# Kernel optimization log

Hardware: AMD Instinct MI355X
Metric: run time of the kernel (lower is better)

The kernel has to match this reference:

```python
import jax, jax.numpy as jnp
import numpy as np

N_ATOMS = 50000
N_PAIRS = 1000000
F = 64   # per-atom features
G = 16   # radial basis functions
V = 32   # vector features
H1 = 128
IN_F = F + V + 1 + V  # 129, non-first interaction module
OUT_F = F + 2


def setup_inputs() -> dict:
    key = jax.random.key(0)
    ks = jax.random.split(key, 12)
    return {
        "atomic_embedding": jax.random.normal(ks[0], (N_ATOMS, F), dtype=jnp.float32),
        "partial_charges": jax.random.normal(ks[1], (N_ATOMS, 1), dtype=jnp.float32),
        "gs": jax.random.uniform(ks[2], (N_PAIRS, G), dtype=jnp.float32),
        "gv": jax.random.normal(ks[3], (N_PAIRS, 3, G), dtype=jnp.float32),
        "agh": jax.random.normal(ks[4], (F, G, V), dtype=jnp.float32) * (1.0 / np.sqrt(G)),
        "W1": jax.random.normal(ks[5], (IN_F, H1), dtype=jnp.float32) * (1.0 / np.sqrt(IN_F)),
        "b1": jnp.zeros((H1,), dtype=jnp.float32),
        "W2": jax.random.normal(ks[6], (H1, H1), dtype=jnp.float32) * (1.0 / np.sqrt(H1)),
        "b2": jnp.zeros((H1,), dtype=jnp.float32),
        "W3": jax.random.normal(ks[7], (H1, OUT_F), dtype=jnp.float32) * (1.0 / np.sqrt(H1)),
        "b3": jnp.zeros((OUT_F,), dtype=jnp.float32),
        "pair_indices": jax.random.randint(ks[8], (2, N_PAIRS), 0, N_ATOMS, dtype=jnp.int64),
    }


def _interaction(atomic_embedding, partial_charges, gs, gv, agh,
                 W1, b1, W2, b2, W3, b3, idx_j):
    n_atoms = atomic_embedding.shape[0]
    v = agh.shape[-1]

    # --- embedding branch ---
    a_j = atomic_embedding[idx_j]                      # (P, F) gather
    # torch: (gs[:,:,None] * a_j[:,None,:]).sum(1) == gs.sum(1, keepdims) * a_j
    avf_s = jnp.einsum('pg,pf->pf', gs, a_j)           # (P, F)
    radial_emb = jax.ops.segment_sum(avf_s, idx_j, num_segments=n_atoms)  # (N, F)

    avf_v = jnp.einsum('pa,pdg,agh->phd', a_j, gv, agh)  # (P, V, 3)
    vec_emb = jax.ops.segment_sum(jnp.sum(avf_v * avf_v, axis=-1),
                                  idx_j, num_segments=n_atoms)            # (N, V)

    # --- partial-charge branch (agh=None path) ---
    q_j = partial_charges[idx_j]                       # (P, 1)
    avf_s_q = jnp.einsum('pg,pf->pf', gs, q_j)         # (P, 1)
    radial_q = jax.ops.segment_sum(avf_s_q, idx_j, num_segments=n_atoms)  # (N, 1)
    vec_q = jnp.zeros((n_atoms, v), dtype=atomic_embedding.dtype)         # (N, V)

    msg = jnp.concatenate([radial_emb, vec_emb, radial_q, vec_q], axis=1)  # (N, F+V+1+V)

    h = jax.nn.gelu(msg @ W1 + b1, approximate=False)
    h = jax.nn.gelu(h @ W2 + b2, approximate=False)
    out = h @ W3 + b3                                   # (N, F+2)

    delta_q = out[:, 0:1]
    f = out[:, 1:2]
    delta_a = out[:, 2:]
    return delta_a, delta_q, f


def reference(atomic_embedding, partial_charges, gs, gv, agh,
              W1, b1, W2, b2, W3, b3, pair_indices):
    idx_j = pair_indices[1]
    return _interaction(atomic_embedding, partial_charges, gs, gv, agh,
                        W1, b1, W2, b2, W3, b3, idx_j)
```

## Files before the change

### kernel.cpp

```cpp
#include <hip/hip_runtime.h>
#include <math.h>

#define NA 50000
#define NP 1000000
#define OUTF 66
#define SCAN_BLOCKS 196
#define ATB 16
#define TSTR 516


__global__ void k_hist(const int* __restrict__ idxj, int* __restrict__ cnt) {
    int p = blockIdx.x * 256 + threadIdx.x;
    if (p < NP) atomicAdd(&cnt[idxj[p]], 1);
}

__global__ __launch_bounds__(256) void k_scanA(const int* __restrict__ cnt,
                                               int* __restrict__ blkS) {
    __shared__ int sh[256];
    int t = threadIdx.x;
    int i = blockIdx.x * 256 + t;
    sh[t] = (i < NA) ? cnt[i] : 0;
    __syncthreads();
    for (int d = 128; d > 0; d >>= 1) {
        if (t < d) sh[t] += sh[t + d];
        __syncthreads();
    }
    if (t == 0) blkS[blockIdx.x] = sh[0];
}

__global__ __launch_bounds__(256) void k_scanB(int* __restrict__ blkS) {
    __shared__ int sh[256];
    int t = threadIdx.x;
    sh[t] = (t < SCAN_BLOCKS) ? blkS[t] : 0;
    __syncthreads();
    for (int d = 1; d < 256; d <<= 1) {
        int x = (t >= d) ? sh[t - d] : 0;
        __syncthreads();
        sh[t] += x;
        __syncthreads();
    }
    int e = (t == 0) ? 0 : sh[t - 1];
    if (t < SCAN_BLOCKS) blkS[t] = e;
}

__global__ __launch_bounds__(256) void k_scanC(const int* __restrict__ cnt,
                                               const int* __restrict__ blkS,
                                               int* __restrict__ offs,
                                               int* __restrict__ curs) {
    __shared__ int sh[256];
    int t = threadIdx.x;
    int i = blockIdx.x * 256 + t;
    sh[t] = (i < NA) ? cnt[i] : 0;
    __syncthreads();
    for (int d = 1; d < 256; d <<= 1) {
        int x = (t >= d) ? sh[t - d] : 0;
        __syncthreads();
        sh[t] += x;
        __syncthreads();
    }
    int excl = ((t == 0) ? 0 : sh[t - 1]) + blkS[blockIdx.x];
    if (i < NA) { offs[i] = excl; curs[i] = excl; }
}

__global__ void k_scatter(const int* __restrict__ idxj, int* __restrict__ curs,
                          int* __restrict__ sortedP) {
    int p = blockIdx.x * 256 + threadIdx.x;
    if (p < NP) {
        int i = idxj[p];
        int pos = atomicAdd(&curs[i], 1);
        sortedP[pos] = (p << 4) | (i & 15);
    }
}

__global__ __launch_bounds__(256)
void k_atoms(const float* __restrict__ emb,
             const float* __restrict__ agh,
             const float* __restrict__ gs,
             const float* __restrict__ gv,
             const int* __restrict__ sortedP,
             const int* __restrict__ offs,
             float* __restrict__ S,
             float* __restrict__ vec) {
    __shared__ float T_lds[ATB * TSTR];
    __shared__ float embS[ATB * 64];
    __shared__ float vecS[ATB * 33];
    __shared__ float sS[ATB];
    const int t = threadIdx.x;
    const int atom0 = blockIdx.x * ATB;

    for (int k = t; k < ATB * 33; k += 256) vecS[k] = 0.f;
    if (t < ATB) sS[t] = 0.f;
    for (int k = t; k < ATB * 64; k += 256) embS[k] = emb[(size_t)atom0 * 64 + k];
    __syncthreads();

    {
        float acc0[ATB], acc1[ATB];
#pragma unroll
        for (int at = 0; at < ATB; ++at) { acc0[at] = 0.f; acc1[at] = 0.f; }
        const int c0 = t, c1 = t + 256;
        for (int a = 0; a < 64; ++a) {
            float w0 = agh[a * 512 + c0];
            float w1 = agh[a * 512 + c1];
#pragma unroll
            for (int at = 0; at < ATB; ++at) {
                float e = embS[at * 64 + a];
                acc0[at] += e * w0;
                acc1[at] += e * w1;
            }
        }
        const int g0 = c0 >> 5, h0 = c0 & 31;
        const int g1 = c1 >> 5, h1 = c1 & 31;
#pragma unroll
        for (int at = 0; at < ATB; ++at) {
            T_lds[at * TSTR + h0 * 16 + g0] = acc0[at];
            T_lds[at * TSTR + h1 * 16 + g1] = acc1[at];
        }
    }
    __syncthreads();

    const int lane = t & 63;
    const int start = offs[atom0];
    const int end = (blockIdx.x + 1 < 3125) ? offs[atom0 + ATB] : NP;

    for (int kb = start; kb < end; kb += 256) {
        const int k = kb + t;
        const bool ok = (k < end);
        const int pk = ok ? sortedP[k] : 0;
        const int p = ok ? (pk >> 4) : 0;
        const int at = pk & 15;
        const int atm = ok ? at : (64 + lane);

        const int atn = __shfl_xor(atm, 1);
        const bool same = (atn == atm);
        const bool flush = (!same) || ((lane & 1) == 0);

        const float4* gs4 = (const float4*)(gs + (size_t)p * 16);
        float4 sa = gs4[0], sb = gs4[1], sc = gs4[2], sd = gs4[3];
        float gq = (sa.x + sa.y + sa.z + sa.w) + (sb.x + sb.y + sb.z + sb.w) +
                   (sc.x + sc.y + sc.z + sc.w) + (sd.x + sd.y + sd.z + sd.w);
        float gqn = __shfl_xor(gq, 1);
        float gqm = gq + (same ? gqn : 0.f);
        if (ok && flush) atomicAdd(&sS[at], gqm);

        const float* Tb = &T_lds[at * TSTR];
        const float* gvp = gv + (size_t)p * 48;

#pragma unroll 1
        for (int hb = 0; hb < 4; ++hb) {
            float e[8];
#pragma unroll
            for (int x = 0; x < 8; ++x) e[x] = 0.f;

#pragma unroll 1
            for (int d = 0; d < 3; ++d) {
                const float4* gd = (const float4*)(gvp + d * 16);
                float4 g0 = gd[0], g1 = gd[1], g2 = gd[2], g3 = gd[3];
#pragma unroll
                for (int hh = 0; hh < 8; ++hh) {
                    const float4* Tr = (const float4*)(Tb + (hb * 8 + hh) * 16);
                    float4 t0 = Tr[0], t1 = Tr[1], t2 = Tr[2], t3 = Tr[3];
                    float v;
                    v  = g0.x * t0.x; v += g0.y * t0.y;
                    v += g0.z * t0.z; v += g0.w * t0.w;
                    v += g1.x * t1.x; v += g1.y * t1.y;
                    v += g1.z * t1.z; v += g1.w * t1.w;
                    v += g2.x * t2.x; v += g2.y * t2.y;
                    v += g2.z * t2.z; v += g2.w * t2.w;
                    v += g3.x * t3.x; v += g3.y * t3.y;
                    v += g3.z * t3.z; v += g3.w * t3.w;
                    e[hh] += v * v;
                }
            }

#pragma unroll
            for (int hh = 0; hh < 8; ++hh) {
                float en = __shfl_xor(e[hh], 1);
                float em = e[hh] + (same ? en : 0.f);
                if (ok && flush) atomicAdd(&vecS[at * 33 + hb * 8 + hh], em);
            }
        }
    }
    __syncthreads();

    for (int k = t; k < ATB * 32; k += 256) {
        int a = k >> 5, h = k & 31;
        vec[(size_t)(atom0 + a) * 32 + h] = vecS[a * 33 + h];
    }
    if (t < ATB) S[atom0 + t] = sS[t];
}

#define MSTR 132
__global__ __launch_bounds__(256) void k_mlp(const float* __restrict__ emb,
                                             const float* __restrict__ q,
                                             const float* __restrict__ S,
                                             const float* __restrict__ vec,
                                             const float* __restrict__ W1,
                                             const float* __restrict__ b1,
                                             const float* __restrict__ W2,
                                             const float* __restrict__ b2,
                                             const float* __restrict__ W3,
                                             const float* __restrict__ b3,
                                             float* __restrict__ out) {
    __shared__ float bufA[64 * MSTR];
    __shared__ float bufB[64 * MSTR];
    const int t = threadIdx.x;
    const int atom0 = blockIdx.x * 64;

    for (int k = t; k < 64 * 97; k += 256) {
        int a = k / 97, c = k - a * 97;
        int i = atom0 + a;
        float val = 0.f;
        if (i < NA) {
            float s = S[i];
            if (c < 64) val = emb[(size_t)i * 64 + c] * s;
            else if (c < 96) val = vec[(size_t)i * 32 + (c - 64)];
            else val = q[i] * s;
        }
        bufA[a * MSTR + c] = val;
    }
    __syncthreads();

    const int jg = t & 31, ag = t >> 5;
    const int j0 = 4 * jg;
    const int abase = ag * 8;
    float acc[8][4];

    {
        float4 bb = *(const float4*)&b1[j0];
#pragma unroll
        for (int a = 0; a < 8; ++a) {
            acc[a][0] = bb.x; acc[a][1] = bb.y; acc[a][2] = bb.z; acc[a][3] = bb.w;
        }
        for (int k4 = 0; k4 < 96; k4 += 4) {
            float4 w0 = *(const float4*)&W1[(k4 + 0) * 128 + j0];
            float4 w1 = *(const float4*)&W1[(k4 + 1) * 128 + j0];
            float4 w2 = *(const float4*)&W1[(k4 + 2) * 128 + j0];
            float4 w3 = *(const float4*)&W1[(k4 + 3) * 128 + j0];
#pragma unroll
            for (int a = 0; a < 8; ++a) {
                float4 m = *(const float4*)&bufA[(abase + a) * MSTR + k4];
                acc[a][0] += m.x * w0.x + m.y * w1.x + m.z * w2.x + m.w * w3.x;
                acc[a][1] += m.x * w0.y + m.y * w1.y + m.z * w2.y + m.w * w3.y;
                acc[a][2] += m.x * w0.z + m.y * w1.z + m.z * w2.z + m.w * w3.z;
                acc[a][3] += m.x * w0.w + m.y * w1.w + m.z * w2.w + m.w * w3.w;
            }
        }
        {
            float4 w = *(const float4*)&W1[96 * 128 + j0];
#pragma unroll
            for (int a = 0; a < 8; ++a) {
                float m = bufA[(abase + a) * MSTR + 96];
                acc[a][0] += m * w.x; acc[a][1] += m * w.y;
                acc[a][2] += m * w.z; acc[a][3] += m * w.w;
            }
        }
#pragma unroll
        for (int a = 0; a < 8; ++a) {
            float4 o;
            o.x = 0.5f * acc[a][0] * (1.f + erff(acc[a][0] * 0.70710678118654752f));
            o.y = 0.5f * acc[a][1] * (1.f + erff(acc[a][1] * 0.70710678118654752f));
            o.z = 0.5f * acc[a][2] * (1.f + erff(acc[a][2] * 0.70710678118654752f));
            o.w = 0.5f * acc[a][3] * (1.f + erff(acc[a][3] * 0.70710678118654752f));
            *(float4*)&bufB[(abase + a) * MSTR + j0] = o;
        }
    }
    __syncthreads();

    {
        float4 bb = *(const float4*)&b2[j0];
#pragma unroll
        for (int a = 0; a < 8; ++a) {
            acc[a][0] = bb.x; acc[a][1] = bb.y; acc[a][2] = bb.z; acc[a][3] = bb.w;
        }
        for (int k4 = 0; k4 < 128; k4 += 4) {
            float4 w0 = *(const float4*)&W2[(k4 + 0) * 128 + j0];
            float4 w1 = *(const float4*)&W2[(k4 + 1) * 128 + j0];
            float4 w2 = *(const float4*)&W2[(k4 + 2) * 128 + j0];
            float4 w3 = *(const float4*)&W2[(k4 + 3) * 128 + j0];
#pragma unroll
            for (int a = 0; a < 8; ++a) {
                float4 m = *(const float4*)&bufB[(abase + a) * MSTR + k4];
                acc[a][0] += m.x * w0.x + m.y * w1.x + m.z * w2.x + m.w * w3.x;
                acc[a][1] += m.x * w0.y + m.y * w1.y + m.z * w2.y + m.w * w3.y;
                acc[a][2] += m.x * w0.z + m.y * w1.z + m.z * w2.z + m.w * w3.z;
                acc[a][3] += m.x * w0.w + m.y * w1.w + m.z * w2.w + m.w * w3.w;
            }
        }
#pragma unroll
        for (int a = 0; a < 8; ++a) {
            float4 o;
            o.x = 0.5f * acc[a][0] * (1.f + erff(acc[a][0] * 0.70710678118654752f));
            o.y = 0.5f * acc[a][1] * (1.f + erff(acc[a][1] * 0.70710678118654752f));
            o.z = 0.5f * acc[a][2] * (1.f + erff(acc[a][2] * 0.70710678118654752f));
            o.w = 0.5f * acc[a][3] * (1.f + erff(acc[a][3] * 0.70710678118654752f));
            *(float4*)&bufA[(abase + a) * MSTR + j0] = o;
        }
    }
    __syncthreads();

    if (j0 < OUTF) {
#pragma unroll
        for (int a = 0; a < 8; ++a) {
            acc[a][0] = b3[j0];
            acc[a][1] = (j0 + 1 < OUTF) ? b3[j0 + 1] : 0.f;
            acc[a][2] = (j0 + 2 < OUTF) ? b3[j0 + 2] : 0.f;
            acc[a][3] = (j0 + 3 < OUTF) ? b3[j0 + 3] : 0.f;
        }
        for (int k = 0; k < 128; ++k) {
            float w0 = W3[k * OUTF + j0];
            float w1 = (j0 + 1 < OUTF) ? W3[k * OUTF + j0 + 1] : 0.f;
            float w2 = (j0 + 2 < OUTF) ? W3[k * OUTF + j0 + 2] : 0.f;
            float w3 = (j0 + 3 < OUTF) ? W3[k * OUTF + j0 + 3] : 0.f;
#pragma unroll
            for (int a = 0; a < 8; ++a) {
                float m = bufA[(abase + a) * MSTR + k];
                acc[a][0] += m * w0; acc[a][1] += m * w1;
                acc[a][2] += m * w2; acc[a][3] += m * w3;
            }
        }
#pragma unroll
        for (int a = 0; a < 8; ++a) {
            int i = atom0 + abase + a;
            if (i < NA) {
#pragma unroll
                for (int c = 0; c < 4; ++c) {
                    int j = j0 + c;
                    if (j < OUTF) {
                        if (j == 0)
                            out[(size_t)NA * 64 + i] = acc[a][c];
                        else if (j == 1)
                            out[(size_t)NA * 64 + NA + i] = acc[a][c];
                        else
                            out[(size_t)i * 64 + (j - 2)] = acc[a][c];
                    }
                }
            }
        }
    }
}

extern "C" void kernel_launch(void* const* d_in, const int* in_sizes, int n_in,
                              void* d_out, int out_size, void* d_ws, size_t ws_size,
                              hipStream_t stream) {
    const float* emb = (const float*)d_in[0];
    const float* q   = (const float*)d_in[1];
    const float* gs  = (const float*)d_in[2];
    const float* gv  = (const float*)d_in[3];
    const float* agh = (const float*)d_in[4];
    const float* W1  = (const float*)d_in[5];
    const float* b1  = (const float*)d_in[6];
    const float* W2  = (const float*)d_in[7];
    const float* b2  = (const float*)d_in[8];
    const float* W3  = (const float*)d_in[9];
    const float* b3  = (const float*)d_in[10];
    const int* pairs = (const int*)d_in[11];
    const int* idxj  = pairs + NP;

    int*   cnt     = (int*)d_ws;
    int*   offs    = cnt + NA;
    int*   curs    = offs + NA;
    int*   blkS    = curs + NA;
    int*   sortedP = blkS + 256;
    float* S       = (float*)(sortedP + NP);
    float* vec     = S + NA;

    hipMemsetAsync(cnt, 0, NA * sizeof(int), stream);
    k_hist<<<(NP + 255) / 256, 256, 0, stream>>>(idxj, cnt);
    k_scanA<<<SCAN_BLOCKS, 256, 0, stream>>>(cnt, blkS);
    k_scanB<<<1, 256, 0, stream>>>(blkS);
    k_scanC<<<SCAN_BLOCKS, 256, 0, stream>>>(cnt, blkS, offs, curs);
    k_scatter<<<(NP + 255) / 256, 256, 0, stream>>>(idxj, curs, sortedP);
    k_atoms<<<NA / ATB, 256, 0, stream>>>(emb, agh, gs, gv, sortedP, offs, S, vec);
    k_mlp<<<(NA + 63) / 64, 256, 0, stream>>>(emb, q, S, vec,
                                              W1, b1, W2, b2, W3, b3,
                                              (float*)d_out);
}
```

Measured before the change: 917.1 us.

## Remap pair loop to wave-per-atom with lanes over vector features; move gs sum to scatter

```diff
diff --git a/kernel.cpp b/kernel.cpp
--- a/kernel.cpp
+++ b/kernel.cpp
@@ -62,34 +62,57 @@
     if (i < NA) { offs[i] = excl; curs[i] = excl; }
 }
 
-__global__ void k_scatter(const int* __restrict__ idxj, int* __restrict__ curs,
-                          int* __restrict__ sortedP) {
+__global__ void k_scatter(const int* __restrict__ idxj,
+                          const float* __restrict__ gs,
+                          int* __restrict__ curs,
+                          int* __restrict__ sortedP,
+                          float* __restrict__ S) {
     int p = blockIdx.x * 256 + threadIdx.x;
     if (p < NP) {
         int i = idxj[p];
         int pos = atomicAdd(&curs[i], 1);
         sortedP[pos] = (p << 4) | (i & 15);
-    }
+        const float4* g4 = (const float4*)(gs + (size_t)p * 16);
+        float4 a = g4[0], b = g4[1], c = g4[2], d = g4[3];
+        float gq = (a.x + a.y + a.z + a.w) + (b.x + b.y + b.z + b.w) +
+                   (c.x + c.y + c.z + c.w) + (d.x + d.y + d.z + d.w);
+        atomicAdd(&S[i], gq);
+    }
+}
+
+__device__ __forceinline__ float pair_contrib(const float* __restrict__ gvp,
+                                              const float4 tA, const float4 tB) {
+    const float4 a0 = *(const float4*)(gvp + 0);
+    const float4 a1 = *(const float4*)(gvp + 4);
+    const float4 a2 = *(const float4*)(gvp + 16);
+    const float4 a3 = *(const float4*)(gvp + 20);
+    const float4 a4 = *(const float4*)(gvp + 32);
+    const float4 a5 = *(const float4*)(gvp + 36);
+    float p0 = a0.x * tA.x + a0.y * tA.y + a0.z * tA.z + a0.w * tA.w
+             + a1.x * tB.x + a1.y * tB.y + a1.z * tB.z + a1.w * tB.w;
+    float p1 = a2.x * tA.x + a2.y * tA.y + a2.z * tA.z + a2.w * tA.w
+             + a3.x * tB.x + a3.y * tB.y + a3.z * tB.z + a3.w * tB.w;
+    float p2 = a4.x * tA.x + a4.y * tA.y + a4.z * tA.z + a4.w * tA.w
+             + a5.x * tB.x + a5.y * tB.y + a5.z * tB.z + a5.w * tB.w;
+    float q0 = p0 + __shfl_xor(p0, 32);
+    float q1 = p1 + __shfl_xor(p1, 32);
+    float q2 = p2 + __shfl_xor(p2, 32);
+    return q0 * q0 + q1 * q1 + q2 * q2;
 }
 
 __global__ __launch_bounds__(256)
+__attribute__((amdgpu_waves_per_eu(4, 4)))
 void k_atoms(const float* __restrict__ emb,
              const float* __restrict__ agh,
-             const float* __restrict__ gs,
              const float* __restrict__ gv,
              const int* __restrict__ sortedP,
              const int* __restrict__ offs,
-             float* __restrict__ S,
              float* __restrict__ vec) {
     __shared__ float T_lds[ATB * TSTR];
     __shared__ float embS[ATB * 64];
-    __shared__ float vecS[ATB * 33];
-    __shared__ float sS[ATB];
     const int t = threadIdx.x;
     const int atom0 = blockIdx.x * ATB;
 
-    for (int k = t; k < ATB * 33; k += 256) vecS[k] = 0.f;
-    if (t < ATB) sS[t] = 0.f;
     for (int k = t; k < ATB * 64; k += 256) embS[k] = emb[(size_t)atom0 * 64 + k];
     __syncthreads();
 
@@ -118,75 +141,42 @@
     }
     __syncthreads();
 
+    const int wv = t >> 6;
     const int lane = t & 63;
-    const int start = offs[atom0];
-    const int end = (blockIdx.x + 1 < 3125) ? offs[atom0 + ATB] : NP;
-
-    for (int kb = start; kb < end; kb += 256) {
-        const int k = kb + t;
-        const bool ok = (k < end);
-        const int pk = ok ? sortedP[k] : 0;
-        const int p = ok ? (pk >> 4) : 0;
-        const int at = pk & 15;
-        const int atm = ok ? at : (64 + lane);
-
-        const int atn = __shfl_xor(atm, 1);
-        const bool same = (atn == atm);
-        const bool flush = (!same) || ((lane & 1) == 0);
-
-        const float4* gs4 = (const float4*)(gs + (size_t)p * 16);
-        float4 sa = gs4[0], sb = gs4[1], sc = gs4[2], sd = gs4[3];
-        float gq = (sa.x + sa.y + sa.z + sa.w) + (sb.x + sb.y + sb.z + sb.w) +
-                   (sc.x + sc.y + sc.z + sc.w) + (sd.x + sd.y + sd.z + sd.w);
-        float gqn = __shfl_xor(gq, 1);
-        float gqm = gq + (same ? gqn : 0.f);
-        if (ok && flush) atomicAdd(&sS[at], gqm);
-
-        const float* Tb = &T_lds[at * TSTR];
-        const float* gvp = gv + (size_t)p * 48;
+    const int h = lane & 31;
+    const int half = lane >> 5;
+    const int hb = half * 8;
 
 #pragma unroll 1
-        for (int hb = 0; hb < 4; ++hb) {
-            float e[8];
-#pragma unroll
-            for (int x = 0; x < 8; ++x) e[x] = 0.f;
-
+    for (int aw = 0; aw < 4; ++aw) {
+        const int at = wv * 4 + aw;
+        const int atom = atom0 + at;
+        const float* Tb = &T_lds[at * TSTR + h * 16 + hb];
+        const float4 tA = *(const float4*)(Tb);
+        const float4 tB = *(const float4*)(Tb + 4);
+        float e = 0.f;
+        const int su = __builtin_amdgcn_readfirstlane(offs[atom]);
+        const int eu = __builtin_amdgcn_readfirstlane(
+            (atom + 1 < NA) ? offs[atom + 1] : NP);
+        int k = su;
 #pragma unroll 1
-            for (int d = 0; d < 3; ++d) {
-                const float4* gd = (const float4*)(gvp + d * 16);
-                float4 g0 = gd[0], g1 = gd[1], g2 = gd[2], g3 = gd[3];
-#pragma unroll
-                for (int hh = 0; hh < 8; ++hh) {
-                    const float4* Tr = (const float4*)(Tb + (hb * 8 + hh) * 16);
-                    float4 t0 = Tr[0], t1 = Tr[1], t2 = Tr[2], t3 = Tr[3];
-                    float v;
-                    v  = g0.x * t0.x; v += g0.y * t0.y;
-                    v += g0.z * t0.z; v += g0.w * t0.w;
-                    v += g1.x * t1.x; v += g1.y * t1.y;
-                    v += g1.z * t1.z; v += g1.w * t1.w;
-                    v += g2.x * t2.x; v += g2.y * t2.y;
-                    v += g2.z * t2.z; v += g2.w * t2.w;
-                    v += g3.x * t3.x; v += g3.y * t3.y;
-                    v += g3.z * t3.z; v += g3.w * t3.w;
-                    e[hh] += v * v;
-                }
-            }
-
-#pragma unroll
-            for (int hh = 0; hh < 8; ++hh) {
-                float en = __shfl_xor(e[hh], 1);
-                float em = e[hh] + (same ? en : 0.f);
-                if (ok && flush) atomicAdd(&vecS[at * 33 + hb * 8 + hh], em);
-            }
-        }
-    }
-    __syncthreads();
-
-    for (int k = t; k < ATB * 32; k += 256) {
-        int a = k >> 5, h = k & 31;
-        vec[(size_t)(atom0 + a) * 32 + h] = vecS[a * 33 + h];
-    }
-    if (t < ATB) S[atom0 + t] = sS[t];
+        for (; k + 3 < eu; k += 4) {
+            const int pA = __builtin_amdgcn_readfirstlane(sortedP[k + 0]) >> 4;
+            const int pB = __builtin_amdgcn_readfirstlane(sortedP[k + 1]) >> 4;
+            const int pC = __builtin_amdgcn_readfirstlane(sortedP[k + 2]) >> 4;
+            const int pD = __builtin_amdgcn_readfirstlane(sortedP[k + 3]) >> 4;
+            e += pair_contrib(gv + (size_t)pA * 48 + hb, tA, tB);
+            e += pair_contrib(gv + (size_t)pB * 48 + hb, tA, tB);
+            e += pair_contrib(gv + (size_t)pC * 48 + hb, tA, tB);
+            e += pair_contrib(gv + (size_t)pD * 48 + hb, tA, tB);
+        }
+#pragma unroll 1
+        for (; k < eu; ++k) {
+            const int p = __builtin_amdgcn_readfirstlane(sortedP[k]) >> 4;
+            e += pair_contrib(gv + (size_t)p * 48 + hb, tA, tB);
+        }
+        if (half == 0) vec[(size_t)atom * 32 + h] = e;
+    }
 }
 
 #define MSTR 132
@@ -365,12 +355,13 @@
     float* vec     = S + NA;
 
     hipMemsetAsync(cnt, 0, NA * sizeof(int), stream);
+    hipMemsetAsync(S, 0, NA * sizeof(float), stream);
     k_hist<<<(NP + 255) / 256, 256, 0, stream>>>(idxj, cnt);
     k_scanA<<<SCAN_BLOCKS, 256, 0, stream>>>(cnt, blkS);
     k_scanB<<<1, 256, 0, stream>>>(blkS);
     k_scanC<<<SCAN_BLOCKS, 256, 0, stream>>>(cnt, blkS, offs, curs);
-    k_scatter<<<(NP + 255) / 256, 256, 0, stream>>>(idxj, curs, sortedP);
-    k_atoms<<<NA / ATB, 256, 0, stream>>>(emb, agh, gs, gv, sortedP, offs, S, vec);
+    k_scatter<<<(NP + 255) / 256, 256, 0, stream>>>(idxj, gs, curs, sortedP, S);
+    k_atoms<<<NA / ATB, 256, 0, stream>>>(emb, agh, gv, sortedP, offs, vec);
     k_mlp<<<(NA + 63) / 64, 256, 0, stream>>>(emb, q, S, vec,
                                               W1, b1, W2, b2, W3, b3,
                                               (float*)d_out);
```

Result: no change. 914.7 us (-0.3%).
